# Kernel optimization log

Measured on AMD Instinct MI355X. Metric: run time of the kernel, lower is better.

## Reference

```python
import jax, jax.numpy as jnp
import numpy as np

NUM_CLASSES = 19
EPS = 1e-8  # torch cosine_similarity eps


def setup_inputs() -> dict:
    key = jax.random.key(0)
    k1, k2 = jax.random.split(key)
    inputs = jax.random.normal(k1, (8, 256, 128, 128), dtype=jnp.float32)  # (B, D, H, W)
    targets = jax.random.randint(k2, (8, 128, 128), 0, NUM_CLASSES)        # (B, H, W)
    return {"inputs": inputs, "targets": targets}


def reference(inputs, targets):
    B, D, H, W = inputs.shape
    C = NUM_CLASSES
    # (N, D) pixel embeddings and (N,) labels
    feats = jnp.transpose(inputs, (0, 2, 3, 1)).reshape(-1, D)
    labels = targets.reshape(-1)

    # per-class centroids: sum of embeddings / max(count, 1)  (matches sum_pixel = max(mask.sum(), 1))
    counts = jax.ops.segment_sum(jnp.ones(labels.shape, jnp.float32), labels, num_segments=C)  # (C,)
    sums = jax.ops.segment_sum(feats, labels, num_segments=C)                                   # (C, D)
    centers = sums / jnp.maximum(counts, 1.0)[:, None]
    present = counts > 0  # classes absent from the batch are skipped in both loss terms

    # ---- sim_loss: sum over present classes of mean_{pixels of class i} (1 - cos(center_i, feat)) ----
    cen_px = centers[labels]                                   # (N, D)
    dot = jnp.sum(feats * cen_px, axis=1)
    n_f = jnp.sqrt(jnp.sum(feats * feats, axis=1))
    n_c = jnp.sqrt(jnp.sum(cen_px * cen_px, axis=1))
    cos_px = dot / jnp.maximum(n_f * n_c, EPS)
    per_class = jax.ops.segment_sum(1.0 - cos_px, labels, num_segments=C) / jnp.maximum(counts, 1.0)
    sim_loss = jnp.sum(jnp.where(present, per_class, 0.0))

    # ---- diff_loss: for each present i, mean_j over all C classes of
    #      (1 - cos(center_j, center_i)) if j == i else relu(cos(center_j, center_i)) ----
    n_cen = jnp.sqrt(jnp.sum(centers * centers, axis=1))       # (C,)
    S = (centers @ centers.T) / jnp.maximum(n_cen[:, None] * n_cen[None, :], EPS)  # (C, C)
    eye = jnp.eye(C, dtype=bool)
    per_pair = jnp.where(eye, 1.0 - S, jnp.maximum(S, 0.0))    # row i = losses vs class i
    per_i = jnp.mean(per_pair, axis=1)                          # mean reduction over C rows
    diff_loss = jnp.sum(jnp.where(present, per_i, 0.0))

    return jnp.reshape(diff_loss + sim_loss, (1,))  # torch returns a shape-(1,) tensor
```

## Files before the change

kernel.cpp:

```cpp
#include <hip/hip_runtime.h>
#include <math.h>

#define D_DIM 256
#define HW 16384
#define C 19
#define N_PX 131072
#define EPS 1e-8f

#define S_SC  1048576.0f
#define IS_S  (1.0f/1048576.0f)
#define U_SC  16777216.0f
#define IS_U  (1.0f/16777216.0f)

#define OFF_S    0
#define OFF_U    4864
#define OFF_CNT  9728
#define WS_ZERO  9747

__global__ void k0_zero(int* __restrict__ ws) {
    int i = blockIdx.x * blockDim.x + threadIdx.x;
    if (i < WS_ZERO) ws[i] = 0;
}

__global__ __launch_bounds__(256) void k1_pass(const float* __restrict__ in,
                                               const int* __restrict__ tgt,
                                               int* __restrict__ wsi) {
    __shared__ int sS[C * 257];
    __shared__ int sU[C * 257];
    __shared__ int s_cnt[C];
    __shared__ __align__(16) float s_nfp[128 * 4];
    const int tid = threadIdx.x;
    const int q   = tid & 63;
    const int dq  = tid >> 6;

    for (int i = tid; i < C * 257; i += 256) { sS[i] = 0; sU[i] = 0; }
    if (tid < C) s_cnt[tid] = 0;
    __syncthreads();

    const int px0 = blockIdx.x << 7;
    const int b   = px0 >> 14;
    const int hwq = (px0 & (HW - 1)) + (q << 1);
    const int p   = px0 + (q << 1);
    const int la = tgt[p], lb = tgt[p + 1];
    if (dq == 0) { atomicAdd(&s_cnt[la], 1); atomicAdd(&s_cnt[lb], 1); }

    const float* base = in + (((size_t)(b * D_DIM + (dq << 6))) << 14) + hwq;

    float nfa = 0.f, nfb = 0.f;
    #pragma unroll
    for (int g = 0; g < 8; ++g) {
        float2 v[8];
        #pragma unroll
        for (int j = 0; j < 8; ++j)
            v[j] = *(const float2*)(base + ((size_t)(g * 8 + j) << 14));
        #pragma unroll
        for (int j = 0; j < 8; ++j) {
            const int dd = (dq << 6) + g * 8 + j;
            nfa += v[j].x * v[j].x; nfb += v[j].y * v[j].y;
            atomicAdd(&sS[la * 257 + dd], __float2int_rn(v[j].x * S_SC));
            atomicAdd(&sS[lb * 257 + dd], __float2int_rn(v[j].y * S_SC));
        }
    }
    s_nfp[(q << 3) + dq]     = nfa;
    s_nfp[(q << 3) + 4 + dq] = nfb;
    __syncthreads();

    const float4 na4 = *(const float4*)&s_nfp[q << 3];
    const float4 nb4 = *(const float4*)&s_nfp[(q << 3) + 4];
    const float nfs_a = na4.x + na4.y + na4.z + na4.w;
    const float nfs_b = nb4.x + nb4.y + nb4.z + nb4.w;
    const float sa = nfs_a > 0.f ? U_SC / sqrtf(nfs_a) : 0.f;
    const float sb = nfs_b > 0.f ? U_SC / sqrtf(nfs_b) : 0.f;

    #pragma unroll
    for (int g = 0; g < 8; ++g) {
        float2 v[8];
        #pragma unroll
        for (int j = 0; j < 8; ++j)
            v[j] = *(const float2*)(base + ((size_t)(g * 8 + j) << 14));
        #pragma unroll
        for (int j = 0; j < 8; ++j) {
            const int dd = (dq << 6) + g * 8 + j;
            atomicAdd(&sU[la * 257 + dd], __float2int_rn(v[j].x * sa));
            atomicAdd(&sU[lb * 257 + dd], __float2int_rn(v[j].y * sb));
        }
    }
    __syncthreads();

    for (int i = tid; i < C * 256; i += 256) {
        int c = i >> 8, d = i & 255;
        atomicAdd(&wsi[OFF_S + i], sS[c * 257 + d]);
        atomicAdd(&wsi[OFF_U + i], sU[c * 257 + d]);
    }
    if (tid < C) atomicAdd(&wsi[OFF_CNT + tid], s_cnt[tid]);
}

__global__ __launch_bounds__(512) void k2_final(const int* __restrict__ wsi,
                                                float* __restrict__ out) {
    __shared__ __align__(16) float s_cen[C * 260];
    __shared__ __align__(16) float s_u[C * 260];
    __shared__ float s_nc[C];
    __shared__ float s_cntf[C];
    __shared__ float s_pair[C * C];
    __shared__ float s_sim[C];
    const int tid = threadIdx.x;

    if (tid < C) s_cntf[tid] = (float)wsi[OFF_CNT + tid];
    __syncthreads();
    for (int i = tid; i < C * 256; i += 512) {
        int c = i >> 8, d = i & 255;
        float icnt = 1.f / fmaxf(s_cntf[c], 1.f);
        s_cen[c * 260 + d] = (float)wsi[OFF_S + i] * IS_S * icnt;
        s_u[c * 260 + d]   = (float)wsi[OFF_U + i] * IS_U;
    }
    __syncthreads();
    if (tid < C) {
        float nsq = 0.f;
        for (int d = 0; d < D_DIM; ++d) {
            float x = s_cen[tid * 260 + d];
            nsq += x * x;
        }
        s_nc[tid] = sqrtf(nsq);
    }
    __syncthreads();
    if (tid < C * C) {
        int i = tid / C, j = tid % C;
        const float4* ci = (const float4*)&s_cen[i * 260];
        const float4* cj = (const float4*)&s_cen[j * 260];
        float dot = 0.f;
        #pragma unroll 8
        for (int k = 0; k < 64; ++k) {
            float4 a = ci[k], bb = cj[k];
            dot += a.x * bb.x + a.y * bb.y + a.z * bb.z + a.w * bb.w;
        }
        float S = dot / fmaxf(s_nc[i] * s_nc[j], EPS);
        s_pair[tid] = (i == j) ? (1.f - S) : fmaxf(S, 0.f);
    } else if (tid >= 384 && tid < 384 + C) {
        int i = tid - 384;
        const float4* ci = (const float4*)&s_cen[i * 260];
        const float4* ui = (const float4*)&s_u[i * 260];
        float dot = 0.f;
        #pragma unroll 8
        for (int k = 0; k < 64; ++k) {
            float4 a = ci[k], bb = ui[k];
            dot += a.x * bb.x + a.y * bb.y + a.z * bb.z + a.w * bb.w;
        }
        s_sim[i] = (s_cntf[i] > 0.f)
                 ? (1.f - dot / fmaxf(s_nc[i] * s_cntf[i], EPS)) : 0.f;
    }
    __syncthreads();
    if (tid < C) {
        float row = 0.f;
        for (int j = 0; j < C; ++j) row += s_pair[tid * C + j];
        s_pair[tid * C] = (s_cntf[tid] > 0.f) ? (row * (1.f / (float)C)) : 0.f;
    }
    __syncthreads();
    if (tid == 0) {
        float tot = 0.f;
        for (int i = 0; i < C; ++i) tot += s_pair[i * C] + s_sim[i];
        out[0] = tot;
    }
}

extern "C" void kernel_launch(void* const* d_in, const int* in_sizes, int n_in,
                              void* d_out, int out_size, void* d_ws, size_t ws_size,
                              hipStream_t stream) {
    const float* in  = (const float*)d_in[0];
    const int*   tgt = (const int*)d_in[1];
    float* out = (float*)d_out;
    int*   wsi = (int*)d_ws;

    k0_zero<<<39, 256, 0, stream>>>(wsi);
    k1_pass<<<1024, 256, 0, stream>>>(in, tgt, wsi);
    k2_final<<<1, 512, 0, stream>>>(wsi, out);
}
```

Before: 242.0 us.

## Halve pass blocks, fuse S/U atomics per pass, and reduce partials via separate kernel

```diff
diff --git a/kernel.cpp b/kernel.cpp
--- a/kernel.cpp
+++ b/kernel.cpp
@@ -15,7 +15,10 @@
 #define OFF_S    0
 #define OFF_U    4864
 #define OFF_CNT  9728
-#define WS_ZERO  9747
+#define WS_ZERO  9760
+#define OFF_PART 9760
+#define PSTRIDE  9760
+#define G1       512
 
 __global__ void k0_zero(int* __restrict__ ws) {
     int i = blockIdx.x * blockDim.x + threadIdx.x;
@@ -37,62 +40,84 @@
     if (tid < C) s_cnt[tid] = 0;
     __syncthreads();
 
-    const int px0 = blockIdx.x << 7;
+    const int px0 = blockIdx.x << 8;
     const int b   = px0 >> 14;
-    const int hwq = (px0 & (HW - 1)) + (q << 1);
-    const int p   = px0 + (q << 1);
-    const int la = tgt[p], lb = tgt[p + 1];
-    if (dq == 0) { atomicAdd(&s_cnt[la], 1); atomicAdd(&s_cnt[lb], 1); }
-
-    const float* base = in + (((size_t)(b * D_DIM + (dq << 6))) << 14) + hwq;
-
-    float nfa = 0.f, nfb = 0.f;
+
     #pragma unroll
-    for (int g = 0; g < 8; ++g) {
-        float2 v[8];
+    for (int r = 0; r < 2; ++r) {
+        const int hwq = (px0 & (HW - 1)) + (r << 7) + (q << 1);
+        const int p   = px0 + (r << 7) + (q << 1);
+        const int la = tgt[p], lb = tgt[p + 1];
+        if (dq == 0) { atomicAdd(&s_cnt[la], 1); atomicAdd(&s_cnt[lb], 1); }
+
+        const float* base = in + (((size_t)(b * D_DIM + (dq << 6))) << 14) + hwq;
+
+        float nfa = 0.f, nfb = 0.f;
         #pragma unroll
-        for (int j = 0; j < 8; ++j)
-            v[j] = *(const float2*)(base + ((size_t)(g * 8 + j) << 14));
+        for (int g = 0; g < 8; ++g) {
+            float2 v[8];
+            #pragma unroll
+            for (int j = 0; j < 8; ++j)
+                v[j] = *(const float2*)(base + ((size_t)(g * 8 + j) << 14));
+            #pragma unroll
+            for (int j = 0; j < 8; ++j) {
+                nfa += v[j].x * v[j].x; nfb += v[j].y * v[j].y;
+            }
+        }
+        s_nfp[(q << 3) + dq]     = nfa;
+        s_nfp[(q << 3) + 4 + dq] = nfb;
+        __syncthreads();
+
+        const float4 na4 = *(const float4*)&s_nfp[q << 3];
+        const float4 nb4 = *(const float4*)&s_nfp[(q << 3) + 4];
+        const float nfs_a = na4.x + na4.y + na4.z + na4.w;
+        const float nfs_b = nb4.x + nb4.y + nb4.z + nb4.w;
+        const float sa = nfs_a > 0.f ? U_SC / sqrtf(nfs_a) : 0.f;
+        const float sb = nfs_b > 0.f ? U_SC / sqrtf(nfs_b) : 0.f;
+
         #pragma unroll
-        for (int j = 0; j < 8; ++j) {
-            const int dd = (dq << 6) + g * 8 + j;
-            nfa += v[j].x * v[j].x; nfb += v[j].y * v[j].y;
-            atomicAdd(&sS[la * 257 + dd], __float2int_rn(v[j].x * S_SC));
-            atomicAdd(&sS[lb * 257 + dd], __float2int_rn(v[j].y * S_SC));
-        }
-    }
-    s_nfp[(q << 3) + dq]     = nfa;
-    s_nfp[(q << 3) + 4 + dq] = nfb;
-    __syncthreads();
-
-    const float4 na4 = *(const float4*)&s_nfp[q << 3];
-    const float4 nb4 = *(const float4*)&s_nfp[(q << 3) + 4];
-    const float nfs_a = na4.x + na4.y + na4.z + na4.w;
-    const float nfs_b = nb4.x + nb4.y + nb4.z + nb4.w;
-    const float sa = nfs_a > 0.f ? U_SC / sqrtf(nfs_a) : 0.f;
-    const float sb = nfs_b > 0.f ? U_SC / sqrtf(nfs_b) : 0.f;
-
-    #pragma unroll
-    for (int g = 0; g < 8; ++g) {
-        float2 v[8];
-        #pragma unroll
-        for (int j = 0; j < 8; ++j)
-            v[j] = *(const float2*)(base + ((size_t)(g * 8 + j) << 14));
-        #pragma unroll
-        for (int j = 0; j < 8; ++j) {
-            const int dd = (dq << 6) + g * 8 + j;
-            atomicAdd(&sU[la * 257 + dd], __float2int_rn(v[j].x * sa));
-            atomicAdd(&sU[lb * 257 + dd], __float2int_rn(v[j].y * sb));
-        }
-    }
-    __syncthreads();
-
+        for (int g = 0; g < 8; ++g) {
+            float2 v[8];
+            #pragma unroll
+            for (int j = 0; j < 8; ++j)
+                v[j] = *(const float2*)(base + ((size_t)(g * 8 + j) << 14));
+            #pragma unroll
+            for (int j = 0; j < 8; ++j) {
+                const int dd = (dq << 6) + g * 8 + j;
+                atomicAdd(&sS[la * 257 + dd], __float2int_rn(v[j].x * S_SC));
+                atomicAdd(&sS[lb * 257 + dd], __float2int_rn(v[j].y * S_SC));
+                atomicAdd(&sU[la * 257 + dd], __float2int_rn(v[j].x * sa));
+                atomicAdd(&sU[lb * 257 + dd], __float2int_rn(v[j].y * sb));
+            }
+        }
+        __syncthreads();
+    }
+
+    int* __restrict__ row = wsi + OFF_PART + (size_t)blockIdx.x * PSTRIDE;
     for (int i = tid; i < C * 256; i += 256) {
         int c = i >> 8, d = i & 255;
-        atomicAdd(&wsi[OFF_S + i], sS[c * 257 + d]);
-        atomicAdd(&wsi[OFF_U + i], sU[c * 257 + d]);
-    }
-    if (tid < C) atomicAdd(&wsi[OFF_CNT + tid], s_cnt[tid]);
+        row[OFF_S + i] = sS[c * 257 + d];
+        row[OFF_U + i] = sU[c * 257 + d];
+    }
+    if (tid < C)                 row[OFF_CNT + tid] = s_cnt[tid];
+    else if (tid < 32)           row[OFF_CNT + tid] = 0;
+}
+
+__global__ __launch_bounds__(256) void k1b_reduce(int* __restrict__ wsi) {
+    const int col4 = blockIdx.x * 256 + threadIdx.x;
+    if (col4 >= PSTRIDE / 4) return;
+    const int4* base = (const int4*)(wsi + OFF_PART)
+                     + (size_t)blockIdx.y * 16 * (PSTRIDE / 4) + col4;
+    int4 acc = {0, 0, 0, 0};
+    #pragma unroll
+    for (int r = 0; r < 16; ++r) {
+        int4 v = base[(size_t)r * (PSTRIDE / 4)];
+        acc.x += v.x; acc.y += v.y; acc.z += v.z; acc.w += v.w;
+    }
+    atomicAdd(&wsi[col4 * 4 + 0], acc.x);
+    atomicAdd(&wsi[col4 * 4 + 1], acc.y);
+    atomicAdd(&wsi[col4 * 4 + 2], acc.z);
+    atomicAdd(&wsi[col4 * 4 + 3], acc.w);
 }
 
 __global__ __launch_bounds__(512) void k2_final(const int* __restrict__ wsi,
@@ -171,6 +196,7 @@
     int*   wsi = (int*)d_ws;
 
     k0_zero<<<39, 256, 0, stream>>>(wsi);
-    k1_pass<<<1024, 256, 0, stream>>>(in, tgt, wsi);
+    k1_pass<<<G1, 256, 0, stream>>>(in, tgt, wsi);
+    k1b_reduce<<<dim3(10, 32), 256, 0, stream>>>(wsi);
     k2_final<<<1, 512, 0, stream>>>(wsi, out);
 }
```

Result: faster. 229.6 us (-5.1%).

## Split norm pass from accumulation and replace global atomics with partial-row reduction

Applied to the files above, without the earlier changes.

```diff
diff --git a/kernel.cpp b/kernel.cpp
--- a/kernel.cpp
+++ b/kernel.cpp
@@ -12,40 +12,40 @@
 #define U_SC  16777216.0f
 #define IS_U  (1.0f/16777216.0f)
 
-#define OFF_S    0
-#define OFF_U    4864
-#define OFF_CNT  9728
-#define WS_ZERO  9747
+#define OFF_S     0
+#define OFF_U     4864
+#define OFF_CNT   9728
+#define WS_ZERO   9747
+#define OFF_INORM 9760
+#define OFF_PART  141312
+#define PROW      2432
 
 __global__ void k0_zero(int* __restrict__ ws) {
     int i = blockIdx.x * blockDim.x + threadIdx.x;
     if (i < WS_ZERO) ws[i] = 0;
 }
 
-__global__ __launch_bounds__(256) void k1_pass(const float* __restrict__ in,
+__global__ __launch_bounds__(256) void kA_norm(const float* __restrict__ in,
                                                const int* __restrict__ tgt,
                                                int* __restrict__ wsi) {
-    __shared__ int sS[C * 257];
-    __shared__ int sU[C * 257];
+    __shared__ __align__(16) float s_nfp[64 * 8];
     __shared__ int s_cnt[C];
-    __shared__ __align__(16) float s_nfp[128 * 4];
     const int tid = threadIdx.x;
     const int q   = tid & 63;
     const int dq  = tid >> 6;
-
-    for (int i = tid; i < C * 257; i += 256) { sS[i] = 0; sU[i] = 0; }
     if (tid < C) s_cnt[tid] = 0;
     __syncthreads();
 
     const int px0 = blockIdx.x << 7;
     const int b   = px0 >> 14;
-    const int hwq = (px0 & (HW - 1)) + (q << 1);
     const int p   = px0 + (q << 1);
-    const int la = tgt[p], lb = tgt[p + 1];
-    if (dq == 0) { atomicAdd(&s_cnt[la], 1); atomicAdd(&s_cnt[lb], 1); }
-
-    const float* base = in + (((size_t)(b * D_DIM + (dq << 6))) << 14) + hwq;
-
+    if (dq == 0) {
+        atomicAdd(&s_cnt[tgt[p]], 1);
+        atomicAdd(&s_cnt[tgt[p + 1]], 1);
+    }
+
+    const float* base = in + (((size_t)(b * D_DIM + (dq << 6))) << 14)
+                           + (px0 & (HW - 1)) + (q << 1);
     float nfa = 0.f, nfb = 0.f;
     #pragma unroll
     for (int g = 0; g < 8; ++g) {
@@ -55,44 +55,99 @@
             v[j] = *(const float2*)(base + ((size_t)(g * 8 + j) << 14));
         #pragma unroll
         for (int j = 0; j < 8; ++j) {
-            const int dd = (dq << 6) + g * 8 + j;
             nfa += v[j].x * v[j].x; nfb += v[j].y * v[j].y;
-            atomicAdd(&sS[la * 257 + dd], __float2int_rn(v[j].x * S_SC));
-            atomicAdd(&sS[lb * 257 + dd], __float2int_rn(v[j].y * S_SC));
         }
     }
     s_nfp[(q << 3) + dq]     = nfa;
     s_nfp[(q << 3) + 4 + dq] = nfb;
     __syncthreads();
 
-    const float4 na4 = *(const float4*)&s_nfp[q << 3];
-    const float4 nb4 = *(const float4*)&s_nfp[(q << 3) + 4];
-    const float nfs_a = na4.x + na4.y + na4.z + na4.w;
-    const float nfs_b = nb4.x + nb4.y + nb4.z + nb4.w;
-    const float sa = nfs_a > 0.f ? U_SC / sqrtf(nfs_a) : 0.f;
-    const float sb = nfs_b > 0.f ? U_SC / sqrtf(nfs_b) : 0.f;
+    if (tid < 64) {
+        const float4 na4 = *(const float4*)&s_nfp[tid << 3];
+        const float4 nb4 = *(const float4*)&s_nfp[(tid << 3) + 4];
+        const float na = na4.x + na4.y + na4.z + na4.w;
+        const float nb = nb4.x + nb4.y + nb4.z + nb4.w;
+        float2 io;
+        io.x = na > 0.f ? U_SC / sqrtf(na) : 0.f;
+        io.y = nb > 0.f ? U_SC / sqrtf(nb) : 0.f;
+        *(float2*)((float*)wsi + OFF_INORM + px0 + (tid << 1)) = io;
+    }
+    if (tid < C) atomicAdd(&wsi[OFF_CNT + tid], s_cnt[tid]);
+}
+
+__global__ __launch_bounds__(256) void kB_accum(const float* __restrict__ in,
+                                                const int* __restrict__ tgt,
+                                                int* __restrict__ wsi) {
+    __shared__ int sS[C * 65];
+    __shared__ int sU[C * 65];
+    const int tid = threadIdx.x;
+    const int q   = tid & 63;
+    const int dq  = tid >> 6;
+    for (int i = tid; i < C * 65; i += 256) { sS[i] = 0; sU[i] = 0; }
+    __syncthreads();
+
+    const int px0   = blockIdx.x << 8;
+    const int slice = blockIdx.y;
+    const int b     = px0 >> 14;
+    const float* inormf = (const float*)wsi + OFF_INORM;
 
     #pragma unroll
-    for (int g = 0; g < 8; ++g) {
-        float2 v[8];
+    for (int r = 0; r < 2; ++r) {
+        const int p  = px0 + (r << 7) + (q << 1);
+        const int la = tgt[p], lb = tgt[p + 1];
+        const float2 io = *(const float2*)(inormf + p);
+        const float* base = in
+            + (((size_t)(b * D_DIM + (slice << 6) + (dq << 4))) << 14)
+            + (px0 & (HW - 1)) + (r << 7) + (q << 1);
+
         #pragma unroll
-        for (int j = 0; j < 8; ++j)
-            v[j] = *(const float2*)(base + ((size_t)(g * 8 + j) << 14));
-        #pragma unroll
-        for (int j = 0; j < 8; ++j) {
-            const int dd = (dq << 6) + g * 8 + j;
-            atomicAdd(&sU[la * 257 + dd], __float2int_rn(v[j].x * sa));
-            atomicAdd(&sU[lb * 257 + dd], __float2int_rn(v[j].y * sb));
-        }
-    }
-    __syncthreads();
-
-    for (int i = tid; i < C * 256; i += 256) {
-        int c = i >> 8, d = i & 255;
-        atomicAdd(&wsi[OFF_S + i], sS[c * 257 + d]);
-        atomicAdd(&wsi[OFF_U + i], sU[c * 257 + d]);
-    }
-    if (tid < C) atomicAdd(&wsi[OFF_CNT + tid], s_cnt[tid]);
+        for (int g = 0; g < 2; ++g) {
+            float2 v[8];
+            #pragma unroll
+            for (int j = 0; j < 8; ++j)
+                v[j] = *(const float2*)(base + ((size_t)(g * 8 + j) << 14));
+            #pragma unroll
+            for (int j = 0; j < 8; ++j) {
+                const int ds = (dq << 4) + g * 8 + j;
+                atomicAdd(&sS[la * 65 + ds], __float2int_rn(v[j].x * S_SC));
+                atomicAdd(&sS[lb * 65 + ds], __float2int_rn(v[j].y * S_SC));
+                atomicAdd(&sU[la * 65 + ds], __float2int_rn(v[j].x * io.x));
+                atomicAdd(&sU[lb * 65 + ds], __float2int_rn(v[j].y * io.y));
+            }
+        }
+    }
+    __syncthreads();
+
+    int* __restrict__ row = wsi + OFF_PART + (size_t)(slice * 512 + blockIdx.x) * PROW;
+    for (int i = tid; i < C * 64; i += 256) {
+        int c = i >> 6, ds = i & 63;
+        row[i]           = sS[c * 65 + ds];
+        row[C * 64 + i]  = sU[c * 65 + ds];
+    }
+}
+
+__global__ __launch_bounds__(256) void k1b_reduce(int* __restrict__ wsi) {
+    const int c4 = blockIdx.x * 256 + threadIdx.x;
+    if (c4 >= PROW / 4) return;
+    const int slice = blockIdx.y >> 4;
+    const int rg    = blockIdx.y & 15;
+    const int4* base = (const int4*)(wsi + OFF_PART)
+                     + ((size_t)slice * 512 + rg * 32) * (PROW / 4) + c4;
+    int4 acc = {0, 0, 0, 0};
+    #pragma unroll
+    for (int r = 0; r < 32; ++r) {
+        int4 v = base[(size_t)r * (PROW / 4)];
+        acc.x += v.x; acc.y += v.y; acc.z += v.z; acc.w += v.w;
+    }
+    const int isU = c4 >= 304;
+    const int j   = c4 - (isU ? 304 : 0);
+    const int c   = j >> 4;
+    const int dd4 = j & 15;
+    int* dst = wsi + (isU ? OFF_U : OFF_S) + c * D_DIM + (slice << 6) + (dd4 << 2);
+    atomicAdd(dst + 0, acc.x);
+    atomicAdd(dst + 1, acc.y);
+    atomicAdd(dst + 2, acc.z);
+    atomicAdd(dst + 3, acc.w);
 }
 
 __global__ __launch_bounds__(512) void k2_final(const int* __restrict__ wsi,
@@ -171,6 +226,8 @@
     int*   wsi = (int*)d_ws;
 
     k0_zero<<<39, 256, 0, stream>>>(wsi);
-    k1_pass<<<1024, 256, 0, stream>>>(in, tgt, wsi);
+    kA_norm<<<1024, 256, 0, stream>>>(in, tgt, wsi);
+    kB_accum<<<dim3(512, 4), 256, 0, stream>>>(in, tgt, wsi);
+    k1b_reduce<<<dim3(3, 64), 256, 0, stream>>>(wsi);
     k2_final<<<1, 512, 0, stream>>>(wsi, out);
 }
```

Result: no change. 239.8 us (-0.9%).

## Split pixel pass into dimension-sliced stream kernels with privatized LDS histograms

Applied to the files above, without the earlier changes.

```diff
diff --git a/kernel.cpp b/kernel.cpp
--- a/kernel.cpp
+++ b/kernel.cpp
@@ -4,95 +4,177 @@
 #define D_DIM 256
 #define HW 16384
 #define C 19
-#define N_PX 131072
 #define EPS 1e-8f
 
-#define S_SC  1048576.0f
-#define IS_S  (1.0f/1048576.0f)
-#define U_SC  16777216.0f
-#define IS_U  (1.0f/16777216.0f)
-
-#define OFF_S    0
-#define OFF_U    4864
-#define OFF_CNT  9728
-#define WS_ZERO  9747
-
-__global__ void k0_zero(int* __restrict__ ws) {
-    int i = blockIdx.x * blockDim.x + threadIdx.x;
-    if (i < WS_ZERO) ws[i] = 0;
-}
-
-__global__ __launch_bounds__(256) void k1_pass(const float* __restrict__ in,
-                                               const int* __restrict__ tgt,
-                                               int* __restrict__ wsi) {
-    __shared__ int sS[C * 257];
-    __shared__ int sU[C * 257];
-    __shared__ int s_cnt[C];
-    __shared__ __align__(16) float s_nfp[128 * 4];
-    const int tid = threadIdx.x;
-    const int q   = tid & 63;
-    const int dq  = tid >> 6;
-
-    for (int i = tid; i < C * 257; i += 256) { sS[i] = 0; sU[i] = 0; }
-    if (tid < C) s_cnt[tid] = 0;
-    __syncthreads();
-
-    const int px0 = blockIdx.x << 7;
-    const int b   = px0 >> 14;
-    const int hwq = (px0 & (HW - 1)) + (q << 1);
-    const int p   = px0 + (q << 1);
-    const int la = tgt[p], lb = tgt[p + 1];
-    if (dq == 0) { atomicAdd(&s_cnt[la], 1); atomicAdd(&s_cnt[lb], 1); }
-
-    const float* base = in + (((size_t)(b * D_DIM + (dq << 6))) << 14) + hwq;
-
-    float nfa = 0.f, nfb = 0.f;
-    #pragma unroll
-    for (int g = 0; g < 8; ++g) {
-        float2 v[8];
-        #pragma unroll
-        for (int j = 0; j < 8; ++j)
-            v[j] = *(const float2*)(base + ((size_t)(g * 8 + j) << 14));
-        #pragma unroll
-        for (int j = 0; j < 8; ++j) {
-            const int dd = (dq << 6) + g * 8 + j;
-            nfa += v[j].x * v[j].x; nfb += v[j].y * v[j].y;
-            atomicAdd(&sS[la * 257 + dd], __float2int_rn(v[j].x * S_SC));
-            atomicAdd(&sS[lb * 257 + dd], __float2int_rn(v[j].y * S_SC));
-        }
-    }
-    s_nfp[(q << 3) + dq]     = nfa;
-    s_nfp[(q << 3) + 4 + dq] = nfb;
-    __syncthreads();
-
-    const float4 na4 = *(const float4*)&s_nfp[q << 3];
-    const float4 nb4 = *(const float4*)&s_nfp[(q << 3) + 4];
-    const float nfs_a = na4.x + na4.y + na4.z + na4.w;
-    const float nfs_b = nb4.x + nb4.y + nb4.z + nb4.w;
-    const float sa = nfs_a > 0.f ? U_SC / sqrtf(nfs_a) : 0.f;
-    const float sb = nfs_b > 0.f ? U_SC / sqrtf(nfs_b) : 0.f;
-
-    #pragma unroll
-    for (int g = 0; g < 8; ++g) {
-        float2 v[8];
-        #pragma unroll
-        for (int j = 0; j < 8; ++j)
-            v[j] = *(const float2*)(base + ((size_t)(g * 8 + j) << 14));
-        #pragma unroll
-        for (int j = 0; j < 8; ++j) {
-            const int dd = (dq << 6) + g * 8 + j;
-            atomicAdd(&sU[la * 257 + dd], __float2int_rn(v[j].x * sa));
-            atomicAdd(&sU[lb * 257 + dd], __float2int_rn(v[j].y * sb));
-        }
-    }
-    __syncthreads();
-
-    for (int i = tid; i < C * 256; i += 256) {
-        int c = i >> 8, d = i & 255;
-        atomicAdd(&wsi[OFF_S + i], sS[c * 257 + d]);
-        atomicAdd(&wsi[OFF_U + i], sU[c * 257 + d]);
-    }
-    if (tid < C) atomicAdd(&wsi[OFF_CNT + tid], s_cnt[tid]);
+#define S_SC 1048576.0f
+#define IS_S (1.0f/1048576.0f)
+#define U_SC 16777216.0f
+#define IS_U (1.0f/16777216.0f)
+
+#define OFF_S      0
+#define OFF_U      4864
+#define OFF_CNT    9728
+#define OFF_IO     9760
+#define OFF_PNF    140832
+#define PNF_STRIDE 8256
+#define OFF_PS     4367904
+#define OFF_PU     4445728
+
+__global__ __launch_bounds__(256) void kA_stream(const float* __restrict__ in,
+                                                 const int* __restrict__ tgt,
+                                                 int* __restrict__ wsi) {
+    __shared__ int sS[8 * 161];
+    const int tid = threadIdx.x;
+    const int bid = blockIdx.x;
+    const int b = bid >> 6, s = (bid >> 1) & 31, h = bid & 1;
+    const int copy = tid & 7;
+    for (int i = tid; i < 8 * 161; i += 256) sS[i] = 0;
+    __syncthreads();
+
+    const int hwb = (h << 13) + (tid << 2);
+    const int pb  = (b << 14) + hwb;
+    int4 lab[8];
+    #pragma unroll
+    for (int it = 0; it < 8; ++it) lab[it] = *(const int4*)(tgt + pb + (it << 10));
+
+    const float* base = in + (((size_t)((b << 8) + (s << 3))) << 14) + hwb;
+    float4 nf[8];
+    #pragma unroll
+    for (int it = 0; it < 8; ++it) nf[it] = make_float4(0.f, 0.f, 0.f, 0.f);
+
+    #pragma unroll
+    for (int d = 0; d < 8; ++d) {
+        float4 v[8];
+        #pragma unroll
+        for (int it = 0; it < 8; ++it)
+            v[it] = *(const float4*)(base + ((size_t)d << 14) + (it << 10));
+        const int sb = copy * 161 + d * 20;
+        #pragma unroll
+        for (int it = 0; it < 8; ++it) {
+            nf[it].x += v[it].x * v[it].x; nf[it].y += v[it].y * v[it].y;
+            nf[it].z += v[it].z * v[it].z; nf[it].w += v[it].w * v[it].w;
+            atomicAdd(&sS[sb + lab[it].x], __float2int_rn(v[it].x * S_SC));
+            atomicAdd(&sS[sb + lab[it].y], __float2int_rn(v[it].y * S_SC));
+            atomicAdd(&sS[sb + lab[it].z], __float2int_rn(v[it].z * S_SC));
+            atomicAdd(&sS[sb + lab[it].w], __float2int_rn(v[it].w * S_SC));
+        }
+    }
+
+    float* pnf = (float*)wsi + OFF_PNF
+               + (size_t)(((b << 1) + h) * 32 + s) * PNF_STRIDE;
+    #pragma unroll
+    for (int it = 0; it < 8; ++it)
+        *(float4*)(pnf + (it << 10) + (tid << 2)) = nf[it];
+
+    __syncthreads();
+    if (tid < 152) {
+        const int d = tid / 19, l = tid - d * 19;
+        int acc = 0;
+        #pragma unroll
+        for (int c = 0; c < 8; ++c) acc += sS[c * 161 + d * 20 + l];
+        wsi[OFF_PS + bid * 152 + tid] = acc;
+    }
+}
+
+__global__ __launch_bounds__(256) void kA2_io(int* __restrict__ wsi) {
+    float* wsf = (float*)wsi;
+    const int j = blockIdx.x, tid = threadIdx.x;
+    const int b = j >> 4, h = (j >> 3) & 1, ch = j & 7;
+    const float* pn = wsf + OFF_PNF + (size_t)((b << 1) + h) * 32 * PNF_STRIDE
+                    + (ch << 10) + (tid << 2);
+    float4 acc = {0.f, 0.f, 0.f, 0.f};
+    #pragma unroll 8
+    for (int s = 0; s < 32; ++s) {
+        float4 v = *(const float4*)(pn + (size_t)s * PNF_STRIDE);
+        acc.x += v.x; acc.y += v.y; acc.z += v.z; acc.w += v.w;
+    }
+    float4 io;
+    io.x = acc.x > 0.f ? U_SC * rsqrtf(acc.x) : 0.f;
+    io.y = acc.y > 0.f ? U_SC * rsqrtf(acc.y) : 0.f;
+    io.z = acc.z > 0.f ? U_SC * rsqrtf(acc.z) : 0.f;
+    io.w = acc.w > 0.f ? U_SC * rsqrtf(acc.w) : 0.f;
+    *(float4*)(wsf + OFF_IO + (b << 14) + (h << 13) + (ch << 10) + (tid << 2)) = io;
+    if (j == 0 && tid < 32) wsi[OFF_CNT + tid] = 0;
+}
+
+__global__ __launch_bounds__(256) void kB_stream(const float* __restrict__ in,
+                                                 const int* __restrict__ tgt,
+                                                 int* __restrict__ wsi) {
+    __shared__ int sU[8 * 161];
+    __shared__ int sH[8 * 21];
+    const int tid = threadIdx.x;
+    const int bid = blockIdx.x;
+    const int b = bid >> 6, s = (bid >> 1) & 31, h = bid & 1;
+    const int copy = tid & 7;
+    for (int i = tid; i < 8 * 161; i += 256) sU[i] = 0;
+    if (tid < 8 * 21) sH[tid] = 0;
+    __syncthreads();
+
+    const int hwb = (h << 13) + (tid << 2);
+    const int pb  = (b << 14) + hwb;
+    const float* iof = (const float*)wsi + OFF_IO;
+    int4   lab[8];
+    float4 io4[8];
+    #pragma unroll
+    for (int it = 0; it < 8; ++it) {
+        lab[it] = *(const int4*)(tgt + pb + (it << 10));
+        io4[it] = *(const float4*)(iof + pb + (it << 10));
+    }
+    if (s == 0) {
+        #pragma unroll
+        for (int it = 0; it < 8; ++it) {
+            atomicAdd(&sH[copy * 21 + lab[it].x], 1);
+            atomicAdd(&sH[copy * 21 + lab[it].y], 1);
+            atomicAdd(&sH[copy * 21 + lab[it].z], 1);
+            atomicAdd(&sH[copy * 21 + lab[it].w], 1);
+        }
+    }
+
+    const float* base = in + (((size_t)((b << 8) + (s << 3))) << 14) + hwb;
+    #pragma unroll
+    for (int d = 0; d < 8; ++d) {
+        float4 v[8];
+        #pragma unroll
+        for (int it = 0; it < 8; ++it)
+            v[it] = *(const float4*)(base + ((size_t)d << 14) + (it << 10));
+        const int sb = copy * 161 + d * 20;
+        #pragma unroll
+        for (int it = 0; it < 8; ++it) {
+            atomicAdd(&sU[sb + lab[it].x], __float2int_rn(v[it].x * io4[it].x));
+            atomicAdd(&sU[sb + lab[it].y], __float2int_rn(v[it].y * io4[it].y));
+            atomicAdd(&sU[sb + lab[it].z], __float2int_rn(v[it].z * io4[it].z));
+            atomicAdd(&sU[sb + lab[it].w], __float2int_rn(v[it].w * io4[it].w));
+        }
+    }
+    __syncthreads();
+    if (tid < 152) {
+        const int d = tid / 19, l = tid - d * 19;
+        int acc = 0;
+        #pragma unroll
+        for (int c = 0; c < 8; ++c) acc += sU[c * 161 + d * 20 + l];
+        wsi[OFF_PU + bid * 152 + tid] = acc;
+    }
+    if (s == 0 && tid < C) {
+        int t = 0;
+        #pragma unroll
+        for (int c = 0; c < 8; ++c) t += sH[c * 21 + tid];
+        atomicAdd(&wsi[OFF_CNT + tid], t);
+    }
+}
+
+__global__ __launch_bounds__(256) void k1b_merge(int* __restrict__ wsi) {
+    const int a = blockIdx.x >> 5, s = blockIdx.x & 31;
+    const int tid = threadIdx.x;
+    if (tid >= 152) return;
+    const int* src = wsi + (a ? OFF_PU : OFF_PS);
+    int acc = 0;
+    #pragma unroll
+    for (int r = 0; r < 16; ++r) {
+        const int row = ((r >> 1) << 6) + (s << 1) + (r & 1);
+        acc += src[row * 152 + tid];
+    }
+    const int d = tid / 19, l = tid - (tid / 19) * 19;
+    wsi[(a ? OFF_U : OFF_S) + l * D_DIM + (s << 3) + d] = acc;
 }
 
 __global__ __launch_bounds__(512) void k2_final(const int* __restrict__ wsi,
@@ -170,7 +252,9 @@
     float* out = (float*)d_out;
     int*   wsi = (int*)d_ws;
 
-    k0_zero<<<39, 256, 0, stream>>>(wsi);
-    k1_pass<<<1024, 256, 0, stream>>>(in, tgt, wsi);
+    kA_stream<<<512, 256, 0, stream>>>(in, tgt, wsi);
+    kA2_io<<<128, 256, 0, stream>>>(wsi);
+    kB_stream<<<512, 256, 0, stream>>>(in, tgt, wsi);
+    k1b_merge<<<64, 256, 0, stream>>>(wsi);
     k2_final<<<1, 512, 0, stream>>>(wsi, out);
 }
```

Result: faster. 229.6 us (-5.1%).
